# Optimization experiments

Measured on AMD Instinct MI355X. Metric: run time of the kernel, lower is better.

## Reference

```python
import jax, jax.numpy as jnp
import numpy as np

N, F, S, D = 8, 16, 196, 1024
H = 8
HD = D // H
L = 1 + F * S  # global feature token + f*s patch tokens


def _ln(x, g, b, eps=1e-5):
    m = x.mean(-1, keepdims=True)
    v = ((x - m) ** 2).mean(-1, keepdims=True)
    return (x - m) / jnp.sqrt(v + eps) * g + b


def _attn(q, k, v, hd):
    s = jnp.einsum('bqd,bkd->bqk', q, k) / jnp.sqrt(jnp.asarray(hd, q.dtype))
    return jnp.einsum('bqk,bkd->bqd', jax.nn.softmax(s, axis=-1), v)


def setup_inputs() -> dict:
    key = jax.random.key(0)
    ks = jax.random.split(key, 8)
    sc = 0.02
    return {
        'x': jax.random.normal(ks[0], (N, L, D), jnp.float32),
        'W_in': jax.random.normal(ks[1], (D, D), jnp.float32) * sc,
        'b_in': jnp.zeros((D,), jnp.float32),
        'g_in': jnp.ones((D,), jnp.float32),
        'beta_in': jnp.zeros((D,), jnp.float32),
        'W_q': jax.random.normal(ks[2], (D, D), jnp.float32) * sc,
        'W_k': jax.random.normal(ks[3], (D, D), jnp.float32) * sc,
        'W_v': jax.random.normal(ks[4], (D, D), jnp.float32) * sc,
        'g_out': jnp.ones((D,), jnp.float32),
        'beta_out': jnp.zeros((D,), jnp.float32),
        'W_out': jax.random.normal(ks[5], (D, D), jnp.float32) * sc,
        'b_out': jnp.zeros((D,), jnp.float32),
        'att_type': 1,  # 1 == 'time', 0 == 'space' (static)
    }


def reference(x, W_in, b_in, g_in, beta_in, W_q, W_k, W_v, g_out, beta_out, W_out, b_out, att_type):
    n = x.shape[0]
    nh = n * H
    # in_fc: Linear + LayerNorm
    x = _ln(x @ W_in + b_in, g_in, beta_in)
    q, k, v = x @ W_q, x @ W_k, x @ W_v

    def split_heads(y):  # [n, L, D] -> [n*h, L, hd]
        return y.reshape(n, L, H, HD).transpose(0, 2, 1, 3).reshape(nh, L, HD)

    q, k, v = map(split_heads, (q, k, v))
    feat_q, q = q[:, :1], q[:, 1:]
    feat_k, k = k[:, :1], k[:, 1:]
    feat_v, v = v[:, :1], v[:, 1:]

    # token_att is computed in the original but never used (dead code):
    # token_att = _attn(feat_q, k, v, HD)

    if att_type == 1:  # time attention: windows of length F per spatial site
        qt = q.reshape(nh, F, S, HD).transpose(0, 2, 1, 3).reshape(nh * S, F, HD)
        kt = k.reshape(nh, F, S, HD).transpose(0, 2, 1, 3).reshape(nh * S, F, HD)
        vt = v.reshape(nh, F, S, HD).transpose(0, 2, 1, 3).reshape(nh * S, F, HD)
        fk = jnp.tile(feat_k, (S, 1, 1))  # torch .repeat(s,1,1)
        fv = jnp.tile(feat_v, (S, 1, 1))
        kk = jnp.concatenate((fk, kt), axis=1)  # [nh*s, 1+f, hd]
        vv = jnp.concatenate((fv, vt), axis=1)
        seq = _attn(qt, kk, vv, HD)  # [nh*s, f, hd]
        seq = seq.reshape(nh, S, F, HD).transpose(0, 2, 1, 3).reshape(nh, F * S, HD)
    else:  # space attention: windows of length S per frame
        qs = q.reshape(nh * F, S, HD)
        ks_ = k.reshape(nh * F, S, HD)
        vs = v.reshape(nh * F, S, HD)
        fk = jnp.tile(feat_k, (F, 1, 1))
        fv = jnp.tile(feat_v, (F, 1, 1))
        kk = jnp.concatenate((fk, ks_), axis=1)  # [nh*f, 1+s, hd]
        vv = jnp.concatenate((fv, vs), axis=1)
        seq = _attn(qs, kk, vv, HD)  # [nh*f, s, hd]
        seq = seq.reshape(nh, F * S, HD)

    out = jnp.concatenate((feat_q, seq), axis=1)  # [nh, L, hd]
    out = out.reshape(n, H, L, HD).transpose(0, 2, 1, 3).reshape(n, L, D)
    out = _ln(out, g_out, beta_out) @ W_out + b_out
    return out
```

## Files before the change

kernel.cpp:

```cpp
#include <hip/hip_runtime.h>
#include <stdint.h>

#define N_B 8
#define F_T 16
#define S_T 196
#define D_M 1024
#define H_N 8
#define HD  128
#define L_T 3137
#define M_R (N_B * L_T)
#define M_P 25216

typedef __attribute__((ext_vector_type(8))) short bf16x8;
typedef __attribute__((ext_vector_type(4))) float f32x4;

__device__ __forceinline__ float b2f(unsigned int u) {
  union { unsigned int i; float f; } x; x.i = u << 16; return x.f;
}
__device__ __forceinline__ unsigned short f2b(float f) {
  union { float f; unsigned int i; } x; x.f = f;
  unsigned int r = x.i + 0x7fffu + ((x.i >> 16) & 1u);
  return (unsigned short)(r >> 16);
}

__global__ __launch_bounds__(256) void convert_pad(const float* __restrict__ x,
                                                   unsigned short* __restrict__ xb,
                                                   int nreal) {
  int i = (blockIdx.x * 256 + threadIdx.x) * 4;
  float4 v;
  if (i < nreal) v = *(const float4*)(x + i);
  else { v.x = 0.f; v.y = 0.f; v.z = 0.f; v.w = 0.f; }
  ushort4 o;
  o.x = f2b(v.x); o.y = f2b(v.y); o.z = f2b(v.z); o.w = f2b(v.w);
  *(ushort4*)(xb + i) = o;
}

struct WP { const float* s[5]; unsigned short* d[5]; };
__global__ __launch_bounds__(256) void transpose5(WP p) {
  __shared__ float t[32][33];
  const int w = blockIdx.z;
  const float* W = p.s[w];
  unsigned short* Wt = p.d[w];
  const int tx = threadIdx.x, ty = threadIdx.y;
  const int n0 = blockIdx.x * 32, k0 = blockIdx.y * 32;
#pragma unroll
  for (int i = 0; i < 4; i++)
    t[ty + i * 8][tx] = W[(size_t)(k0 + ty + i * 8) * D_M + n0 + tx];
  __syncthreads();
#pragma unroll
  for (int i = 0; i < 4; i++)
    Wt[(size_t)(n0 + ty + i * 8) * D_M + k0 + tx] = f2b(t[tx][ty + i * 8]);
}

__device__ __forceinline__ void async16(const unsigned short* g, unsigned short* l) {
  __builtin_amdgcn_global_load_lds((const __attribute__((address_space(1))) void*)g,
                                   (__attribute__((address_space(3))) void*)l, 16, 0, 0);
}

struct Outs { void* p[3]; };

template <int MODE>
__global__ __launch_bounds__(256) void gemm_bt(const unsigned short* __restrict__ A,
                                               const unsigned short* __restrict__ Bt,
                                               const float* __restrict__ bias,
                                               Outs o, int Mreal) {
  constexpr int NCB = (MODE == 3) ? 24 : 8;
  __shared__ __align__(16) unsigned short lds[17408];
  unsigned short* As = lds;
  unsigned short* Bs = lds + 4096;
  const int tid = threadIdx.x;
  const int lane = tid & 63;
  const int wv = tid >> 6;
  const int wm = wv >> 1, wn = wv & 1;

  const int flat = blockIdx.y * NCB + blockIdx.x;
  int rowBase, colBase;
  if (MODE == 3) {
    const int lin = (flat & 7) * 591 + (flat >> 3);
    rowBase = (lin / 24) * 128; colBase = (lin % 24) * 128;
  } else {
    const int lin = (flat & 7) * 197 + (flat >> 3);
    rowBase = (lin >> 3) * 128; colBase = (lin & 7) * 128;
  }

  const int c0 = 2 * wv, c1 = c0 + 1;
  const int srow = lane >> 2;
  const int sg = lane & 3;
  const int gk = ((sg ^ (srow & 3)) * 8);
  const unsigned short* gA0 = A + (size_t)(rowBase + c0 * 16 + srow) * 1024 + gk;
  const unsigned short* gA1 = A + (size_t)(rowBase + c1 * 16 + srow) * 1024 + gk;
  const unsigned short* gB0 = Bt + (size_t)(colBase + c0 * 16 + srow) * 1024 + gk;
  const unsigned short* gB1 = Bt + (size_t)(colBase + c1 * 16 + srow) * 1024 + gk;
  unsigned short* lA0 = As + c0 * 512;
  unsigned short* lA1 = As + c1 * 512;
  unsigned short* lB0 = Bs + c0 * 512;
  unsigned short* lB1 = Bs + c1 * 512;

  f32x4 acc[4][4] = {};

  const int mf = lane & 15, kg = lane >> 4;
  const int slot = (kg ^ (mf & 3)) * 8;
  const unsigned short* Ar = As + (wm * 64 + mf) * 32 + slot;
  const unsigned short* Br = Bs + (wn * 64 + mf) * 32 + slot;

  for (int kt = 0; kt < 1024; kt += 32) {
    __syncthreads();
    async16(gA0 + kt, lA0);
    async16(gA1 + kt, lA1);
    async16(gB0 + kt, lB0);
    async16(gB1 + kt, lB1);
    __syncthreads();
    bf16x8 av[4], bv[4];
#pragma unroll
    for (int i = 0; i < 4; i++) av[i] = *(const bf16x8*)(Ar + i * 16 * 32);
#pragma unroll
    for (int j = 0; j < 4; j++) bv[j] = *(const bf16x8*)(Br + j * 16 * 32);
#pragma unroll
    for (int i = 0; i < 4; i++)
#pragma unroll
      for (int j = 0; j < 4; j++)
        acc[i][j] = __builtin_amdgcn_mfma_f32_16x16x32_bf16(av[i], bv[j], acc[i][j], 0, 0, 0);
  }

  __syncthreads();
  if (MODE == 2) {
    float* Cf = (float*)lds;
    float* outF = (float*)o.p[0];
#pragma unroll
    for (int p = 0; p < 2; p++) {
      if (p) __syncthreads();
      if (wm == p) {
#pragma unroll
        for (int j = 0; j < 4; j++) {
          const int col_l = wn * 64 + j * 16 + mf;
          const float bval = bias[colBase + col_l];
#pragma unroll
          for (int i = 0; i < 4; i++)
#pragma unroll
            for (int r = 0; r < 4; r++)
              Cf[(i * 16 + kg * 4 + r) * 132 + col_l] = acc[i][j][r] + bval;
        }
      }
      __syncthreads();
#pragma unroll
      for (int t = 0; t < 8; t++) {
        const int g = t * 256 + tid;
        const int row = g >> 5, ch = g & 31;
        const int grow = rowBase + p * 64 + row;
        if (grow < Mreal)
          *(float4*)(outF + (size_t)grow * 1024 + colBase + ch * 4) =
              *(const float4*)(Cf + row * 132 + ch * 4);
      }
    }
  } else {
    unsigned short* Cs = lds;
#pragma unroll
    for (int j = 0; j < 4; j++) {
      const int col_l = wn * 64 + j * 16 + mf;
      const float bval = (MODE == 1) ? bias[colBase + col_l] : 0.f;
#pragma unroll
      for (int i = 0; i < 4; i++)
#pragma unroll
        for (int r = 0; r < 4; r++)
          Cs[(wm * 64 + i * 16 + kg * 4 + r) * 136 + col_l] = f2b(acc[i][j][r] + bval);
    }
    __syncthreads();
    unsigned short* C;
    int cb;
    if (MODE == 3) { C = (unsigned short*)o.p[colBase >> 10]; cb = colBase & 1023; }
    else { C = (unsigned short*)o.p[0]; cb = colBase; }
#pragma unroll
    for (int t = 0; t < 8; t++) {
      const int g = t * 256 + tid;
      const int row = g >> 4, ch = g & 15;
      *(uint4*)(C + (size_t)(rowBase + row) * 1024 + cb + ch * 8) =
          *(const uint4*)(Cs + row * 136 + ch * 8);
    }
  }
}

__global__ __launch_bounds__(256) void ln_kernel(const unsigned short* __restrict__ src,
                                                 const unsigned short* __restrict__ src0,
                                                 const float* __restrict__ g,
                                                 const float* __restrict__ beta,
                                                 unsigned short* __restrict__ out, int Mreal) {
  const int row = blockIdx.x, tid = threadIdx.x;
  unsigned short* op = out + (size_t)row * 1024 + tid * 4;
  if (row >= Mreal) {
    ushort4 z; z.x = 0; z.y = 0; z.z = 0; z.w = 0;
    *(ushort4*)op = z;
    return;
  }
  const unsigned short* s = src;
  if (src0 != nullptr && (row % L_T) == 0) s = src0;
  const unsigned short* ip = s + (size_t)row * 1024 + tid * 4;
  uint2 raw = *(const uint2*)ip;
  float x0 = b2f(raw.x & 0xffffu), x1 = b2f(raw.x >> 16);
  float x2 = b2f(raw.y & 0xffffu), x3 = b2f(raw.y >> 16);
  float sum = x0 + x1 + x2 + x3;
  float sq = x0 * x0 + x1 * x1 + x2 * x2 + x3 * x3;
#pragma unroll
  for (int off = 32; off > 0; off >>= 1) {
    sum += __shfl_down(sum, off);
    sq += __shfl_down(sq, off);
  }
  __shared__ float red[8];
  if ((tid & 63) == 0) { red[tid >> 6] = sum; red[4 + (tid >> 6)] = sq; }
  __syncthreads();
  const float ts = red[0] + red[1] + red[2] + red[3];
  const float tq = red[4] + red[5] + red[6] + red[7];
  const float mean = ts * (1.f / 1024.f);
  const float var = tq * (1.f / 1024.f) - mean * mean;
  const float rstd = rsqrtf(var + 1e-5f);
  const float4 gv = *(const float4*)(g + tid * 4);
  const float4 bv = *(const float4*)(beta + tid * 4);
  ushort4 o;
  o.x = f2b((x0 - mean) * rstd * gv.x + bv.x);
  o.y = f2b((x1 - mean) * rstd * gv.y + bv.y);
  o.z = f2b((x2 - mean) * rstd * gv.z + bv.z);
  o.w = f2b((x3 - mean) * rstd * gv.w + bv.w);
  *(ushort4*)op = o;
}

#define ATT_T_BLOCKS (64 * 49)
__global__ __launch_bounds__(256) void attn_kernel(const unsigned short* __restrict__ q,
                                                   const unsigned short* __restrict__ k,
                                                   const unsigned short* __restrict__ v,
                                                   unsigned short* __restrict__ out,
                                                   const int* __restrict__ att_type) {
  __shared__ __align__(16) char smem[22528];
  const int tid = threadIdx.x;
  const int bid = blockIdx.x;
  const int at = att_type[0];

  if (at == 1) {
    if (bid >= ATT_T_BLOCKS) return;
    const int lane = tid & 63, wv = tid >> 6;
    const int l15 = lane & 15, kg = lane >> 4;
    const int hb = bid / 49, sb = bid - hb * 49;
    const int s = sb * 4 + wv;
    const int n = hb >> 3, h = hb & 7;
    const int fi = (hb * S_T + s) & 63;
    const size_t frow = (size_t)(fi >> 3) * L_T;
    const int fcol = (fi & 7) * HD;
    const int qbase = n * L_T + 1 + s;
    const int hcol = h * HD;

    unsigned short* Pl = (unsigned short*)(smem + wv * 5632);
    unsigned short* Vl = (unsigned short*)(smem + wv * 5632 + 1024);

    {
      const int dim0 = l15 * 8;
#pragma unroll
      for (int p = 0; p < 5; p++) {
        const int key = p * 4 + kg;
        if (key < 17) {
          const unsigned short* vp = (key == 0)
              ? (v + frow * 1024 + fcol + dim0)
              : (v + (size_t)(qbase + (key - 1) * S_T) * 1024 + hcol + dim0);
          uint4 r = *(const uint4*)vp;
          unsigned int* wp = (unsigned int*)Vl + key * 65 + l15 * 4;
          wp[0] = r.x; wp[1] = r.y; wp[2] = r.z; wp[3] = r.w;
        }
      }
    }

    bf16x8 aq[4], bk0[4], bk1[4];
    {
      const unsigned short* qp = q + (size_t)(qbase + l15 * S_T) * 1024 + hcol + kg * 8;
      const unsigned short* kp = (l15 == 0)
          ? (k + frow * 1024 + fcol + kg * 8)
          : (k + (size_t)(qbase + (l15 - 1) * S_T) * 1024 + hcol + kg * 8);
      const unsigned short* kp1 = k + (size_t)(qbase + 15 * S_T) * 1024 + hcol + kg * 8;
#pragma unroll
      for (int t = 0; t < 4; t++) {
        aq[t] = *(const bf16x8*)(qp + t * 32);
        bk0[t] = *(const bf16x8*)(kp + t * 32);
        if (l15 == 0) bk1[t] = *(const bf16x8*)(kp1 + t * 32);
        else {
          bf16x8 z = {};
          bk1[t] = z;
        }
      }
    }

    f32x4 c0 = {}, c1 = {};
#pragma unroll
    for (int t = 0; t < 4; t++) {
      c0 = __builtin_amdgcn_mfma_f32_16x16x32_bf16(aq[t], bk0[t], c0, 0, 0, 0);
      c1 = __builtin_amdgcn_mfma_f32_16x16x32_bf16(aq[t], bk1[t], c1, 0, 0, 0);
    }

    const float scl = 0.08838834764831845f;
#pragma unroll
    for (int r = 0; r < 4; r++) {
      float v0 = c0[r] * scl;
      float k16 = __shfl(c1[r] * scl, lane & 48);
      float mx = v0;
#pragma unroll
      for (int m = 1; m < 16; m <<= 1) mx = fmaxf(mx, __shfl_xor(mx, m));
      mx = fmaxf(mx, k16);
      float p = __expf(v0 - mx);
      float p16 = __expf(k16 - mx);
      float sum = p;
#pragma unroll
      for (int m = 1; m < 16; m <<= 1) sum += __shfl_xor(sum, m);
      sum += p16;
      const float inv = 1.f / sum;
      const int row = kg * 4 + r;
      Pl[row * 32 + l15] = f2b(p * inv);
      Pl[row * 32 + 16 + l15] = (l15 == 0) ? f2b(p16 * inv) : (unsigned short)0;
    }

    bf16x8 ap = *(const bf16x8*)(Pl + l15 * 32 + kg * 8);
#pragma unroll
    for (int nt = 0; nt < 8; nt++) {
      const int dim = nt * 16 + l15;
      bf16x8 bv;
#pragma unroll
      for (int j = 0; j < 8; j++) {
        const int key = kg * 8 + j;
        const int kc = (key < 17) ? key : 0;
        unsigned short raw = Vl[kc * 130 + dim];
        bv[j] = (key < 17) ? (short)raw : (short)0;
      }
      f32x4 z = {};
      f32x4 o = __builtin_amdgcn_mfma_f32_16x16x32_bf16(ap, bv, z, 0, 0, 0);
#pragma unroll
      for (int r = 0; r < 4; r++) {
        const int qi = kg * 4 + r;
        out[(size_t)(qbase + qi * S_T) * 1024 + hcol + nt * 16 + l15] = f2b(o[r]);
      }
    }
    return;
  }

  float (*qs)[132] = (float (*)[132])smem;
  float (*sc)[212] = (float (*)[212])(smem + 8448);
  const int hb = bid / 208;
  const int rem = bid - hb * 208;
  const int f = rem / 13, qc = rem - f * 13;
  const int n = hb >> 3, h = hb & 7;
  const int fi = (hb * F_T + f) & 63;
  const size_t frow = (size_t)(fi >> 3) * L_T;
  const int fcol = (fi & 7) * HD;
  const int kbase = n * L_T + 1 + f * S_T;
  const int qbase = kbase + qc * 16;
  const int nk = S_T + 1;
  const int nqv = (qc == 12) ? 4 : 16;
  const int hcol = h * HD;

  {
    const int i = tid >> 4, db = (tid & 15) * 8;
    float* dst = &qs[i][db];
    if (i < nqv) {
      const unsigned short* qp = q + (size_t)(qbase + i) * 1024 + hcol + db;
      uint4 r = *(const uint4*)qp;
      dst[0] = b2f(r.x & 0xffffu); dst[1] = b2f(r.x >> 16);
      dst[2] = b2f(r.y & 0xffffu); dst[3] = b2f(r.y >> 16);
      dst[4] = b2f(r.z & 0xffffu); dst[5] = b2f(r.z >> 16);
      dst[6] = b2f(r.w & 0xffffu); dst[7] = b2f(r.w >> 16);
    } else {
#pragma unroll
      for (int u = 0; u < 8; u++) dst[u] = 0.f;
    }
  }
  __syncthreads();

  const int nslot = 16 * nk;
  for (int slot = tid; slot < nslot; slot += 256) {
    const int i = slot / nk, j = slot - i * nk;
    const unsigned short* kp = (j == 0)
        ? (k + frow * 1024 + fcol)
        : (k + (size_t)(kbase + (j - 1)) * 1024 + hcol);
    float acc = 0.f;
#pragma unroll 4
    for (int d = 0; d < 128; d += 8) {
      uint4 r = *(const uint4*)(kp + d);
      acc += qs[i][d + 0] * b2f(r.x & 0xffffu);
      acc += qs[i][d + 1] * b2f(r.x >> 16);
      acc += qs[i][d + 2] * b2f(r.y & 0xffffu);
      acc += qs[i][d + 3] * b2f(r.y >> 16);
      acc += qs[i][d + 4] * b2f(r.z & 0xffffu);
      acc += qs[i][d + 5] * b2f(r.z >> 16);
      acc += qs[i][d + 6] * b2f(r.w & 0xffffu);
      acc += qs[i][d + 7] * b2f(r.w >> 16);
    }
    sc[i][j] = acc * 0.08838834764831845f;
  }
  __syncthreads();

  if (tid < 16) {
    const int i = tid;
    float m = -1e30f;
    for (int j = 0; j < nk; j++) m = fmaxf(m, sc[i][j]);
    float ssum = 0.f;
    for (int j = 0; j < nk; j++) {
      float e = __expf(sc[i][j] - m);
      sc[i][j] = e;
      ssum += e;
    }
    const float inv = 1.f / ssum;
    for (int j = 0; j < nk; j++) sc[i][j] *= inv;
  }
  __syncthreads();

  {
    const int i = tid >> 4, db = (tid & 15) * 8;
    float o[8];
#pragma unroll
    for (int u = 0; u < 8; u++) o[u] = 0.f;
    for (int j = 0; j < nk; j++) {
      const unsigned short* vp = (j == 0)
          ? (v + frow * 1024 + fcol + db)
          : (v + (size_t)(kbase + (j - 1)) * 1024 + hcol + db);
      const float p = sc[i][j];
      uint4 r = *(const uint4*)vp;
      o[0] += p * b2f(r.x & 0xffffu); o[1] += p * b2f(r.x >> 16);
      o[2] += p * b2f(r.y & 0xffffu); o[3] += p * b2f(r.y >> 16);
      o[4] += p * b2f(r.z & 0xffffu); o[5] += p * b2f(r.z >> 16);
      o[6] += p * b2f(r.w & 0xffffu); o[7] += p * b2f(r.w >> 16);
    }
    if (i < nqv) {
      unsigned short* op = out + (size_t)(qbase + i) * 1024 + hcol + db;
      uint4 w;
      w.x = (unsigned)f2b(o[0]) | ((unsigned)f2b(o[1]) << 16);
      w.y = (unsigned)f2b(o[2]) | ((unsigned)f2b(o[3]) << 16);
      w.z = (unsigned)f2b(o[4]) | ((unsigned)f2b(o[5]) << 16);
      w.w = (unsigned)f2b(o[6]) | ((unsigned)f2b(o[7]) << 16);
      *(uint4*)op = w;
    }
  }
}

extern "C" void kernel_launch(void* const* d_in, const int* in_sizes, int n_in,
                              void* d_out, int out_size, void* d_ws, size_t ws_size,
                              hipStream_t stream) {
  const float* x        = (const float*)d_in[0];
  const float* W_in     = (const float*)d_in[1];
  const float* b_in     = (const float*)d_in[2];
  const float* g_in     = (const float*)d_in[3];
  const float* beta_in  = (const float*)d_in[4];
  const float* W_q      = (const float*)d_in[5];
  const float* W_k      = (const float*)d_in[6];
  const float* W_v      = (const float*)d_in[7];
  const float* g_out    = (const float*)d_in[8];
  const float* beta_out = (const float*)d_in[9];
  const float* W_out    = (const float*)d_in[10];
  const float* b_out    = (const float*)d_in[11];
  const int* att_type   = (const int*)d_in[12];
  float* out = (float*)d_out;

  char* ws = (char*)d_ws;
  const size_t MB = (size_t)M_P * 1024 * 2;
  unsigned short* xb = (unsigned short*)(ws + 0 * MB);
  unsigned short* t1 = (unsigned short*)(ws + 1 * MB);
  unsigned short* xh = (unsigned short*)(ws + 2 * MB);
  unsigned short* kb = (unsigned short*)(ws + 3 * MB);
  unsigned short* vb = (unsigned short*)(ws + 4 * MB);
  unsigned short* wt = (unsigned short*)(ws + 5 * MB);
  const size_t WSZ = (size_t)1024 * 1024;
  unsigned short* wt_in  = wt;
  unsigned short* wqkv   = wt + 1 * WSZ;
  unsigned short* wt_out = wt + 4 * WSZ;

  convert_pad<<<M_P, 256, 0, stream>>>(x, xb, M_R * 1024);

  WP wp;
  wp.s[0] = W_in; wp.s[1] = W_q; wp.s[2] = W_k; wp.s[3] = W_v; wp.s[4] = W_out;
  wp.d[0] = wt_in;
  wp.d[1] = wqkv;
  wp.d[2] = wqkv + 1 * WSZ;
  wp.d[3] = wqkv + 2 * WSZ;
  wp.d[4] = wt_out;
  transpose5<<<dim3(32, 32, 5), dim3(32, 8), 0, stream>>>(wp);

  Outs o1; o1.p[0] = t1; o1.p[1] = nullptr; o1.p[2] = nullptr;
  gemm_bt<1><<<dim3(8, 197), 256, 0, stream>>>(xb, wt_in, b_in, o1, M_P);
  ln_kernel<<<M_P, 256, 0, stream>>>(t1, nullptr, g_in, beta_in, xh, M_R);

  Outs oq; oq.p[0] = t1; oq.p[1] = kb; oq.p[2] = vb;
  gemm_bt<3><<<dim3(24, 197), 256, 0, stream>>>(xh, wqkv, nullptr, oq, M_P);

  attn_kernel<<<13312, 256, 0, stream>>>(t1, kb, vb, xb, att_type);
  ln_kernel<<<M_P, 256, 0, stream>>>(xb, t1, g_out, beta_out, xh, M_R);

  Outs oo; oo.p[0] = out; oo.p[1] = nullptr; oo.p[2] = nullptr;
  gemm_bt<2><<<dim3(8, 197), 256, 0, stream>>>(xh, wt_out, b_out, oo, M_R);
}
```

Measured before the change: 637.9 us.

## Double GEMM K-tile to 64 with 8-way swizzle and column-grouped raster

The bf16 GEMM main loop now stages a 64-wide K slice per iteration instead of 32. This halves the number of barrier pairs and gives each sync two MFMA sub-steps. The LDS swizzle is widened to 8 groups to match, and the MODE 3 (QKV, 24 column blocks) tile raster is regrouped into column groups of 8 so blocks sharing B columns run together for better L2 reuse. LDS use per block rises (B tile offset moves to 8192), which could affect occupancy.

```diff
diff --git a/kernel.cpp b/kernel.cpp
--- a/kernel.cpp
+++ b/kernel.cpp
@@ -67,7 +67,7 @@
   constexpr int NCB = (MODE == 3) ? 24 : 8;
   __shared__ __align__(16) unsigned short lds[17408];
   unsigned short* As = lds;
-  unsigned short* Bs = lds + 4096;
+  unsigned short* Bs = lds + 8192;
   const int tid = threadIdx.x;
   const int lane = tid & 63;
   const int wv = tid >> 6;
@@ -77,49 +77,63 @@
   int rowBase, colBase;
   if (MODE == 3) {
     const int lin = (flat & 7) * 591 + (flat >> 3);
-    rowBase = (lin / 24) * 128; colBase = (lin % 24) * 128;
+    const int cg = lin / 1576;
+    const int rem = lin - cg * 1576;
+    rowBase = (rem >> 3) * 128;
+    colBase = (cg * 8 + (rem & 7)) * 128;
   } else {
     const int lin = (flat & 7) * 197 + (flat >> 3);
-    rowBase = (lin >> 3) * 128; colBase = (lin & 7) * 128;
-  }
-
-  const int c0 = 2 * wv, c1 = c0 + 1;
-  const int srow = lane >> 2;
-  const int sg = lane & 3;
-  const int gk = ((sg ^ (srow & 3)) * 8);
-  const unsigned short* gA0 = A + (size_t)(rowBase + c0 * 16 + srow) * 1024 + gk;
-  const unsigned short* gA1 = A + (size_t)(rowBase + c1 * 16 + srow) * 1024 + gk;
-  const unsigned short* gB0 = Bt + (size_t)(colBase + c0 * 16 + srow) * 1024 + gk;
-  const unsigned short* gB1 = Bt + (size_t)(colBase + c1 * 16 + srow) * 1024 + gk;
-  unsigned short* lA0 = As + c0 * 512;
-  unsigned short* lA1 = As + c1 * 512;
-  unsigned short* lB0 = Bs + c0 * 512;
-  unsigned short* lB1 = Bs + c1 * 512;
+    rowBase = (lin >> 3) * 128;
+    colBase = (lin & 7) * 128;
+  }
+
+  const int srow8 = lane >> 3;
+  const int gk = ((lane & 7) ^ srow8) * 8;
+  const unsigned short* gA = A + (size_t)(rowBase + wv * 32 + srow8) * 1024 + gk;
+  const unsigned short* gB = Bt + (size_t)(colBase + wv * 32 + srow8) * 1024 + gk;
+  unsigned short* lA = As + wv * 2048 + lane * 8;
+  unsigned short* lB = Bs + wv * 2048 + lane * 8;
 
   f32x4 acc[4][4] = {};
 
   const int mf = lane & 15, kg = lane >> 4;
-  const int slot = (kg ^ (mf & 3)) * 8;
-  const unsigned short* Ar = As + (wm * 64 + mf) * 32 + slot;
-  const unsigned short* Br = Bs + (wn * 64 + mf) * 32 + slot;
-
-  for (int kt = 0; kt < 1024; kt += 32) {
+  const int sl0 = ((kg) ^ (mf & 7)) * 8;
+  const int sl1 = ((4 + kg) ^ (mf & 7)) * 8;
+  const unsigned short* Ar = As + (wm * 64 + mf) * 64;
+  const unsigned short* Br = Bs + (wn * 64 + mf) * 64;
+
+  for (int kt = 0; kt < 1024; kt += 64) {
     __syncthreads();
-    async16(gA0 + kt, lA0);
-    async16(gA1 + kt, lA1);
-    async16(gB0 + kt, lB0);
-    async16(gB1 + kt, lB1);
+#pragma unroll
+    for (int ii = 0; ii < 4; ii++) {
+      async16(gA + ii * 8 * 1024 + kt, lA + ii * 512);
+      async16(gB + ii * 8 * 1024 + kt, lB + ii * 512);
+    }
     __syncthreads();
-    bf16x8 av[4], bv[4];
-#pragma unroll
-    for (int i = 0; i < 4; i++) av[i] = *(const bf16x8*)(Ar + i * 16 * 32);
-#pragma unroll
-    for (int j = 0; j < 4; j++) bv[j] = *(const bf16x8*)(Br + j * 16 * 32);
-#pragma unroll
-    for (int i = 0; i < 4; i++)
-#pragma unroll
-      for (int j = 0; j < 4; j++)
-        acc[i][j] = __builtin_amdgcn_mfma_f32_16x16x32_bf16(av[i], bv[j], acc[i][j], 0, 0, 0);
+    {
+      bf16x8 av[4], bv[4];
+#pragma unroll
+      for (int i = 0; i < 4; i++) av[i] = *(const bf16x8*)(Ar + i * 1024 + sl0);
+#pragma unroll
+      for (int j = 0; j < 4; j++) bv[j] = *(const bf16x8*)(Br + j * 1024 + sl0);
+#pragma unroll
+      for (int i = 0; i < 4; i++)
+#pragma unroll
+        for (int j = 0; j < 4; j++)
+          acc[i][j] = __builtin_amdgcn_mfma_f32_16x16x32_bf16(av[i], bv[j], acc[i][j], 0, 0, 0);
+    }
+    {
+      bf16x8 av[4], bv[4];
+#pragma unroll
+      for (int i = 0; i < 4; i++) av[i] = *(const bf16x8*)(Ar + i * 1024 + sl1);
+#pragma unroll
+      for (int j = 0; j < 4; j++) bv[j] = *(const bf16x8*)(Br + j * 1024 + sl1);
+#pragma unroll
+      for (int i = 0; i < 4; i++)
+#pragma unroll
+        for (int j = 0; j < 4; j++)
+          acc[i][j] = __builtin_amdgcn_mfma_f32_16x16x32_bf16(av[i], bv[j], acc[i][j], 0, 0, 0);
+    }
   }
 
   __syncthreads();
```

Measured after the change: 615.0 us. 3.6% less time.
